# Kernel optimization log

Hardware: AMD Instinct MI355X
Metric: run time of the kernel (lower is better)

## Reference

```python
import jax, jax.numpy as jnp
import numpy as np

Z_SIZE, KEY_SIZE, HID = 128, 256, 512
NEG = -1e9


def setup_inputs() -> dict:
    key = jax.random.key(0)
    ks = jax.random.split(key, 8)
    B, T, H, W, Y = 512, 32, 32, 32, 4
    D = H * W
    g = lambda k, shape, s: jax.random.normal(k, shape, jnp.float32) * s
    return {
        "x_seq": jax.random.normal(ks[0], (B, T, H, W), jnp.float32),
        # Encoder (conv encoder stand-in: flatten -> MLP -> z_size)
        "enc_w1": g(ks[1], (D, HID), 0.03),
        "enc_b1": jnp.zeros((HID,), jnp.float32),
        "enc_w2": g(ks[2], (HID, Z_SIZE), 0.05),
        "enc_b2": jnp.zeros((Z_SIZE,), jnp.float32),
        # LSTM input kernel (recurrent kernel unused: h_prev is always 0)
        "lstm_Wx": g(ks[3], (KEY_SIZE + 1, 4 * HID), 0.05),
        "lstm_b": jnp.zeros((4 * HID,), jnp.float32),
        "keyw_W": g(ks[4], (HID, KEY_SIZE), 0.05),
        "keyw_b": jnp.zeros((KEY_SIZE,), jnp.float32),
        "g_W": g(ks[5], (HID, 1), 0.05),
        "g_b": jnp.zeros((1,), jnp.float32),
        "y_W": g(ks[6], (HID, Y), 0.05),
        "y_b": jnp.zeros((Y,), jnp.float32),
        "conf_gain": jnp.float32(1.0),
        "conf_bias": jnp.float32(0.0),
    }


def reference(x_seq, enc_w1, enc_b1, enc_w2, enc_b2, lstm_Wx, lstm_b,
              keyw_W, keyw_b, g_W, g_b, y_W, y_b, conf_gain, conf_bias):
    B, T = x_seq.shape[0], x_seq.shape[1]
    Y = y_b.shape[0]
    dt = x_seq.dtype

    # Encode all frames at once: (B, T, Z)
    x_flat = x_seq.reshape(B, T, -1)
    z_seq = jax.nn.relu(x_flat @ enc_w1 + enc_b1) @ enc_w2 + enc_b2
    # Pad with the zero z_t used at the final step t == T  -> (B, T+1, Z)
    z_pad = jnp.concatenate([z_seq, jnp.zeros((B, 1, Z_SIZE), dt)], axis=1)

    def lstm_step(x):  # single keras LSTM step from zero state (h=c=0)
        gates = x @ lstm_Wx + lstm_b
        i, f, c, o = jnp.split(gates, 4, axis=-1)  # keras gate order i,f,c,o
        c_new = jax.nn.sigmoid(i) * jnp.tanh(c)     # f*c_prev = 0
        return jax.nn.sigmoid(o) * jnp.tanh(c_new)

    slot_idx = jnp.arange(T + 1)

    def step(carry, t):
        key_r, M_k, M_v, _ = carry
        z_t = z_pad[:, t]                       # (B, Z)
        h = lstm_step(key_r)                    # (B, HID)
        key_w = h @ keyw_W + keyw_b             # (B, KEY)
        gate = jax.nn.sigmoid(h @ g_W + g_b)    # (B, 1)
        y_lin = h @ y_W + y_b                   # (B, Y)

        # Content-based read over memory slots written so far (slots < t)
        scores = jnp.einsum('bz,btz->bt', z_t, M_v)          # (B, T+1)
        valid = (slot_idx < t)[None, :]
        w_k = jax.nn.softmax(jnp.where(valid, scores, NEG), axis=1)
        c_k = jax.nn.sigmoid(scores * conf_gain + conf_bias)  # (B, T+1)
        Mkc = jnp.concatenate([M_k, c_k[..., None]], axis=-1)  # (B, T+1, KEY+1)
        key_r_new = gate * jnp.einsum('bt,btk->bk', w_k, Mkc)
        key_r_new = jnp.where(t == 0, jnp.zeros_like(key_r_new), key_r_new)

        # Memory write (append == write into preallocated slot t)
        M_k = M_k.at[:, t].set(key_w)
        M_v = M_v.at[:, t].set(z_t)
        return (key_r_new, M_k, M_v, y_lin), None

    init = (jnp.zeros((B, KEY_SIZE + 1), dt),
            jnp.zeros((B, T + 1, KEY_SIZE), dt),
            jnp.zeros((B, T + 1, Z_SIZE), dt),
            jnp.zeros((B, Y), dt))
    (_, _, _, y_pred_linear), _ = jax.lax.scan(step, init, jnp.arange(T + 1))
    y_pred = jnp.argmax(y_pred_linear, axis=1)
    return y_pred_linear, y_pred
```

## Files before the change

### kernel.cpp

```cpp
#include <hip/hip_runtime.h>
#include <math.h>

__device__ __forceinline__ float sigf(float x) { return 1.0f / (1.0f + expf(-x)); }
__device__ __forceinline__ float4 f4fma(float s, float4 b, float4 a) {
  return make_float4(fmaf(s, b.x, a.x), fmaf(s, b.y, a.y), fmaf(s, b.z, a.z), fmaf(s, b.w, a.w));
}
__device__ __forceinline__ void wave_red2(float4& v) {
  v.x += __shfl_xor(v.x, 16); v.y += __shfl_xor(v.y, 16);
  v.z += __shfl_xor(v.z, 16); v.w += __shfl_xor(v.w, 16);
  v.x += __shfl_xor(v.x, 32); v.y += __shfl_xor(v.y, 32);
  v.z += __shfl_xor(v.z, 32); v.w += __shfl_xor(v.w, 32);
}

__global__ __launch_bounds__(256) void k_gemm1(const float* __restrict__ X,
                                               const float* __restrict__ W,
                                               const float* __restrict__ Bv,
                                               float* __restrict__ C)
{
  const int K = 1024, N = 512;
  __shared__ float As[16][132];
  __shared__ float Bs[16][132];
  int tid = threadIdx.x;
  int bm = blockIdx.x >> 2;
  int bn = blockIdx.x & 3;
  int tx = tid & 15, ty = tid >> 4;
  int xr = tid & 127, xc8 = (tid >> 7) * 8;
  int wk = tid >> 4, wc = (tid & 15) * 8;
  const float* Xb = X + (size_t)(bm * 128 + xr) * K;
  const float* Wb = W + bn * 128 + wc;
  float acc[8][8];
#pragma unroll
  for (int i = 0; i < 8; i++)
#pragma unroll
    for (int j = 0; j < 8; j++) acc[i][j] = 0.f;

  for (int k0 = 0; k0 < K; k0 += 16) {
    float4 a0 = *(const float4*)(Xb + k0 + xc8);
    float4 a1 = *(const float4*)(Xb + k0 + xc8 + 4);
    float4 b0 = *(const float4*)(W + (size_t)(k0 + wk) * N + bn * 128 + wc);
    float4 b1 = *(const float4*)(W + (size_t)(k0 + wk) * N + bn * 128 + wc + 4);
    As[xc8 + 0][xr] = a0.x; As[xc8 + 1][xr] = a0.y;
    As[xc8 + 2][xr] = a0.z; As[xc8 + 3][xr] = a0.w;
    As[xc8 + 4][xr] = a1.x; As[xc8 + 5][xr] = a1.y;
    As[xc8 + 6][xr] = a1.z; As[xc8 + 7][xr] = a1.w;
    *(float4*)(&Bs[wk][wc]) = b0;
    *(float4*)(&Bs[wk][wc + 4]) = b1;
    __syncthreads();
#pragma unroll
    for (int kk = 0; kk < 16; kk++) {
      float a[8], b[8];
      *(float4*)(a)     = *(const float4*)(&As[kk][ty * 8]);
      *(float4*)(a + 4) = *(const float4*)(&As[kk][ty * 8 + 4]);
      *(float4*)(b)     = *(const float4*)(&Bs[kk][tx * 4]);
      *(float4*)(b + 4) = *(const float4*)(&Bs[kk][64 + tx * 4]);
#pragma unroll
      for (int i = 0; i < 8; i++)
#pragma unroll
        for (int j = 0; j < 8; j++) acc[i][j] = fmaf(a[i], b[j], acc[i][j]);
    }
    __syncthreads();
  }
  int crow0 = bm * 128 + ty * 8;
  int ccolA = bn * 128 + tx * 4;
  int ccolB = bn * 128 + 64 + tx * 4;
  float4 bvA = *(const float4*)(Bv + ccolA);
  float4 bvB = *(const float4*)(Bv + ccolB);
#pragma unroll
  for (int i = 0; i < 8; i++) {
    float4 vA = make_float4(acc[i][0] + bvA.x, acc[i][1] + bvA.y,
                            acc[i][2] + bvA.z, acc[i][3] + bvA.w);
    float4 vB = make_float4(acc[i][4] + bvB.x, acc[i][5] + bvB.y,
                            acc[i][6] + bvB.z, acc[i][7] + bvB.w);
    vA.x = vA.x > 0.f ? vA.x : 0.f; vA.y = vA.y > 0.f ? vA.y : 0.f;
    vA.z = vA.z > 0.f ? vA.z : 0.f; vA.w = vA.w > 0.f ? vA.w : 0.f;
    vB.x = vB.x > 0.f ? vB.x : 0.f; vB.y = vB.y > 0.f ? vB.y : 0.f;
    vB.z = vB.z > 0.f ? vB.z : 0.f; vB.w = vB.w > 0.f ? vB.w : 0.f;
    *(float4*)(&C[(size_t)(crow0 + i) * N + ccolA]) = vA;
    *(float4*)(&C[(size_t)(crow0 + i) * N + ccolB]) = vB;
  }
}

__global__ __launch_bounds__(256) void k_gemm2(const float* __restrict__ A,
                                               const float* __restrict__ W,
                                               const float* __restrict__ Bv,
                                               float* __restrict__ zp)
{
  const int K = 512, N = 128;
  __shared__ float As[8][132];
  __shared__ float Bs[8][132];
  int tid = threadIdx.x;
  int bm = blockIdx.x;
  int tx = tid & 15, ty = tid >> 4;
  int arow = tid >> 1, acol4 = (tid & 1) * 4;
  int bkk = tid >> 5, bn4 = (tid & 31) * 4;
  const float* Ab = A + (size_t)(bm * 128) * K;
  float acc[8][8];
#pragma unroll
  for (int i = 0; i < 8; i++)
#pragma unroll
    for (int j2 = 0; j2 < 8; j2++) acc[i][j2] = 0.f;
  for (int k0 = 0; k0 < K; k0 += 8) {
    float4 av = *(const float4*)(Ab + (size_t)arow * K + k0 + acol4);
    float4 bv = *(const float4*)(W + (size_t)(k0 + bkk) * N + bn4);
    As[acol4 + 0][arow] = av.x;
    As[acol4 + 1][arow] = av.y;
    As[acol4 + 2][arow] = av.z;
    As[acol4 + 3][arow] = av.w;
    *(float4*)(&Bs[bkk][bn4]) = bv;
    __syncthreads();
#pragma unroll
    for (int kk = 0; kk < 8; kk++) {
      float a[8], b[8];
      *(float4*)(a)     = *(const float4*)(&As[kk][ty * 8]);
      *(float4*)(a + 4) = *(const float4*)(&As[kk][ty * 8 + 4]);
      *(float4*)(b)     = *(const float4*)(&Bs[kk][tx * 8]);
      *(float4*)(b + 4) = *(const float4*)(&Bs[kk][tx * 8 + 4]);
#pragma unroll
      for (int i = 0; i < 8; i++)
#pragma unroll
        for (int j2 = 0; j2 < 8; j2++) acc[i][j2] = fmaf(a[i], b[j2], acc[i][j2]);
    }
    __syncthreads();
  }
  int ccol0 = tx * 8;
#pragma unroll
  for (int i = 0; i < 8; i++) {
    int r = bm * 128 + ty * 8 + i;
    int b = r >> 5, tt = r & 31;
#pragma unroll
    for (int j2 = 0; j2 < 8; j2++) {
      zp[(size_t)b * (33 * 128) + tt * 128 + ccol0 + j2] = acc[i][j2] + Bv[ccol0 + j2];
    }
  }
}

__global__ __launch_bounds__(256) void k_gram(const float* __restrict__ zp,
                                              float* __restrict__ warr,
                                              float* __restrict__ wc,
                                              const float* __restrict__ cgp,
                                              const float* __restrict__ cbp)
{
  __shared__ float zl[32][128];
  __shared__ float sg[32][32];
  int b = blockIdx.x, tid = threadIdx.x;
  const float* zb = zp + (size_t)b * (33 * 128);
  for (int i = tid; i < 32 * 128; i += 256) (&zl[0][0])[i] = zb[i];
  __syncthreads();
  for (int p = tid; p < 496; p += 256) {
    int t = 1;
    while (p >= t * (t + 1) / 2) t++;
    int tp = p - t * (t - 1) / 2;
    const float* za = &zl[t][0];
    const float* zc = &zl[tp][0];
    float s = 0.f;
#pragma unroll 4
    for (int c = 0; c < 128; c += 4) {
      s += za[c] * zc[c] + za[c + 1] * zc[c + 1] + za[c + 2] * zc[c + 2] + za[c + 3] * zc[c + 3];
    }
    sg[t][tp] = s;
  }
  __syncthreads();
  if (tid >= 1 && tid < 32) {
    int t = tid;
    float cg = cgp[0], cb = cbp[0];
    float m = -3.0e38f;
    for (int tp = 0; tp < t; tp++) m = fmaxf(m, sg[t][tp]);
    float se = 0.f;
    for (int tp = 0; tp < t; tp++) se += expf(sg[t][tp] - m);
    float inv = 1.0f / se;
    float wcs = 0.f;
    for (int tp = 0; tp < t; tp++) {
      float s = sg[t][tp];
      float w = expf(s - m) * inv;
      warr[(size_t)b * 1024 + t * 32 + tp] = w;
      wcs = fmaf(w, sigf(fmaf(s, cg, cb)), wcs);
    }
    wc[b * 32 + t] = wcs;
  }
}

__global__ __launch_bounds__(256) void k_gates(const float* __restrict__ Wx,
                                               const float* __restrict__ lb,
                                               const float* __restrict__ keyrT,
                                               float* __restrict__ h, int t)
{
  __shared__ float smem[6656];
  float* As = smem;
  float* Bs = smem + 640;
  float* Rb = smem;
  const int tid = threadIdx.x;
  const int rt = blockIdx.x >> 4;
  const int ct = blockIdx.x & 15;
  const int row0 = rt * 16;
  const int hc0 = ct * 32;

  if (t > 0) {
    const int ksub = tid >> 4;
    const int pos = tid & 15;
    const int rg = pos >> 3;
    const int cg = pos & 7;
    float4 aI[8], aC[8], aO[8];
#pragma unroll
    for (int r = 0; r < 8; r++) {
      aI[r] = make_float4(0.f, 0.f, 0.f, 0.f);
      aC[r] = make_float4(0.f, 0.f, 0.f, 0.f);
      aO[r] = make_float4(0.f, 0.f, 0.f, 0.f);
    }
    for (int c = 0; c < 8; ++c) {
      const int k0 = c * 32;
      if (c) __syncthreads();
      if (tid < 128) {
        const int kkA = tid >> 2, lA = (tid & 3) * 4;
        *(float4*)&As[kkA * 20 + lA] =
            *(const float4*)&keyrT[(size_t)(k0 + kkA) * 512 + row0 + lA];
      }
      {
        const int kkB = tid >> 3, lB = (tid & 7) * 4;
        const float* wrow = Wx + (size_t)(k0 + kkB) * 2048;
        *(float4*)&Bs[kkB * 100 + lB]      = *(const float4*)(wrow + hc0 + lB);
        *(float4*)&Bs[kkB * 100 + 32 + lB] = *(const float4*)(wrow + 1024 + hc0 + lB);
        *(float4*)&Bs[kkB * 100 + 64 + lB] = *(const float4*)(wrow + 1536 + hc0 + lB);
      }
      __syncthreads();
#pragma unroll
      for (int i = 0; i < 2; ++i) {
        const int kk = ksub * 2 + i;
        float a8[8];
        *(float4*)&a8[0] = *(const float4*)&As[kk * 20 + rg * 8];
        *(float4*)&a8[4] = *(const float4*)&As[kk * 20 + rg * 8 + 4];
        float4 bI = *(const float4*)&Bs[kk * 100 + cg * 4];
        float4 bC = *(const float4*)&Bs[kk * 100 + 32 + cg * 4];
        float4 bO = *(const float4*)&Bs[kk * 100 + 64 + cg * 4];
#pragma unroll
        for (int r = 0; r < 8; r++) {
          float a = a8[r];
          aI[r] = f4fma(a, bI, aI[r]);
          aC[r] = f4fma(a, bC, aC[r]);
          aO[r] = f4fma(a, bO, aO[r]);
        }
      }
    }
    if (ksub == 0) {
      float a8[8];
      *(float4*)&a8[0] = *(const float4*)&keyrT[(size_t)256 * 512 + row0 + rg * 8];
      *(float4*)&a8[4] = *(const float4*)&keyrT[(size_t)256 * 512 + row0 + rg * 8 + 4];
      const float* wrow = Wx + (size_t)256 * 2048;
      float4 bI = *(const float4*)(wrow + hc0 + cg * 4);
      float4 bC = *(const float4*)(wrow + 1024 + hc0 + cg * 4);
      float4 bO = *(const float4*)(wrow + 1536 + hc0 + cg * 4);
#pragma unroll
      for (int r = 0; r < 8; r++) {
        float a = a8[r];
        aI[r] = f4fma(a, bI, aI[r]);
        aC[r] = f4fma(a, bC, aC[r]);
        aO[r] = f4fma(a, bO, aO[r]);
      }
    }
#pragma unroll
    for (int r = 0; r < 8; r++) { wave_red2(aI[r]); wave_red2(aC[r]); wave_red2(aO[r]); }
    __syncthreads();
    {
      const int wave = tid >> 6, lane = tid & 63;
      if (lane < 16) {
        float* w = &Rb[wave * 1600 + lane * 100];
#pragma unroll
        for (int r = 0; r < 8; r++) {
          *(float4*)&w[r * 12 + 0] = aI[r];
          *(float4*)&w[r * 12 + 4] = aC[r];
          *(float4*)&w[r * 12 + 8] = aO[r];
        }
      }
    }
    __syncthreads();
    {
      const int r = tid >> 4;
      const int hc2 = (tid & 15) * 2;
      const int p = (r >> 3) * 8 + (hc2 >> 2);
      const int base = p * 100 + (r & 7) * 12;
      const int off = hc2 & 3;
      float sI0 = Rb[base + off]     + Rb[1600 + base + off]     + Rb[3200 + base + off]     + Rb[4800 + base + off];
      float sI1 = Rb[base + off + 1] + Rb[1600 + base + off + 1] + Rb[3200 + base + off + 1] + Rb[4800 + base + off + 1];
      float sC0 = Rb[base + 4 + off]     + Rb[1600 + base + 4 + off]     + Rb[3200 + base + 4 + off]     + Rb[4800 + base + 4 + off];
      float sC1 = Rb[base + 4 + off + 1] + Rb[1600 + base + 4 + off + 1] + Rb[3200 + base + 4 + off + 1] + Rb[4800 + base + 4 + off + 1];
      float sO0 = Rb[base + 8 + off]     + Rb[1600 + base + 8 + off]     + Rb[3200 + base + 8 + off]     + Rb[4800 + base + 8 + off];
      float sO1 = Rb[base + 8 + off + 1] + Rb[1600 + base + 8 + off + 1] + Rb[3200 + base + 8 + off + 1] + Rb[4800 + base + 8 + off + 1];
      float iv0 = sI0 + lb[hc0 + hc2],        iv1 = sI1 + lb[hc0 + hc2 + 1];
      float cv0 = sC0 + lb[1024 + hc0 + hc2], cv1 = sC1 + lb[1024 + hc0 + hc2 + 1];
      float ov0 = sO0 + lb[1536 + hc0 + hc2], ov1 = sO1 + lb[1536 + hc0 + hc2 + 1];
      float h0 = sigf(ov0) * tanhf(sigf(iv0) * tanhf(cv0));
      float h1 = sigf(ov1) * tanhf(sigf(iv1) * tanhf(cv1));
      *(float2*)&h[(size_t)(row0 + r) * 512 + hc0 + hc2] = make_float2(h0, h1);
    }
  } else {
    const int r = tid >> 4;
    const int hc2 = (tid & 15) * 2;
    float iv0 = lb[hc0 + hc2],        iv1 = lb[hc0 + hc2 + 1];
    float cv0 = lb[1024 + hc0 + hc2], cv1 = lb[1024 + hc0 + hc2 + 1];
    float ov0 = lb[1536 + hc0 + hc2], ov1 = lb[1536 + hc0 + hc2 + 1];
    float h0 = sigf(ov0) * tanhf(sigf(iv0) * tanhf(cv0));
    float h1 = sigf(ov1) * tanhf(sigf(iv1) * tanhf(cv1));
    *(float2*)&h[(size_t)(row0 + r) * 512 + hc0 + hc2] = make_float2(h0, h1);
  }
}

__global__ __launch_bounds__(256) void k_update(const float* __restrict__ h,
                                                const float* __restrict__ kW,
                                                const float* __restrict__ kb,
                                                const float* __restrict__ gW,
                                                const float* __restrict__ gb,
                                                const float* __restrict__ warr,
                                                const float* __restrict__ wc,
                                                float* __restrict__ Mk,
                                                float* __restrict__ keyrT, int t)
{
  __shared__ float smem[10640];
  float* hs  = smem;
  float* gWs = smem + 8256;
  float* wws = smem + 8768;
  float* gsh = smem + 9344;
  float* kWs = smem + 9360;
  float* Rb  = smem + 9360;
  const int tid = threadIdx.x;
  const int rt = blockIdx.x >> 4;
  const int ct = blockIdx.x & 15;
  const int row0 = rt * 16;
  const int c0 = ct * 16;

  {
    const int r = tid >> 4, seg = tid & 15;
    const float* hrow = h + (size_t)(row0 + r) * 512 + seg * 32;
    float* hd = hs + r * 516 + seg * 32;
#pragma unroll
    for (int q = 0; q < 8; ++q) {
      const int qp = ((q + seg) & 7) * 4;
      *(float4*)&hd[qp] = *(const float4*)&hrow[qp];
    }
    if (tid < 128) *(float4*)&gWs[tid * 4] = *(const float4*)&gW[tid * 4];
    wws[r * 36 + seg]      = (seg < t)      ? warr[(size_t)(row0 + r) * 1024 + t * 32 + seg] : 0.f;
    wws[r * 36 + 16 + seg] = (16 + seg < t) ? warr[(size_t)(row0 + r) * 1024 + t * 32 + 16 + seg] : 0.f;
  }
  __syncthreads();

  const int ksub = tid >> 4, pu = tid & 15, rgu = pu >> 2, cgu = pu & 3;
  float4 au[4];
#pragma unroll
  for (int r = 0; r < 4; r++) au[r] = make_float4(0.f, 0.f, 0.f, 0.f);
  for (int c = 0; c < 16; ++c) {
    if (c) __syncthreads();
    if (tid < 128) {
      const int kkW = tid >> 2, lW = (tid & 3) * 4;
      *(float4*)&kWs[kkW * 20 + lW] =
          *(const float4*)&kW[(size_t)(c * 32 + kkW) * 256 + c0 + lW];
    }
    __syncthreads();
#pragma unroll
    for (int i = 0; i < 2; ++i) {
      const int kk = ksub * 2 + i;
      float4 b4 = *(const float4*)&kWs[kk * 20 + cgu * 4];
      const int kidx = c * 32 + kk;
#pragma unroll
      for (int jj = 0; jj < 4; ++jj) {
        float a = hs[(rgu * 4 + jj) * 516 + kidx];
        au[jj] = f4fma(a, b4, au[jj]);
      }
    }
  }
#pragma unroll
  for (int r = 0; r < 4; r++) wave_red2(au[r]);
  __syncthreads();
  {
    const int wave = tid >> 6, lane = tid & 63;
    if (lane < 16) {
      float* w = &Rb[wave * 320 + lane * 20];
#pragma unroll
      for (int r = 0; r < 4; r++) *(float4*)&w[r * 4] = au[r];
    }
  }
  __syncthreads();
  {
    const int r = tid >> 4, cc = tid & 15;
    const int p = (r >> 2) * 4 + (cc >> 2);
    const int e = p * 20 + (r & 3) * 4 + (cc & 3);
    float v = Rb[e] + Rb[320 + e] + Rb[640 + e] + Rb[960 + e];
    Mk[(size_t)(row0 + r) * 8192 + t * 256 + c0 + cc] = v + kb[c0 + cc];
  }
  {
    const int r = tid >> 4, seg = tid & 15;
    const float* hp = &hs[r * 516 + seg * 32];
    const float* gp = &gWs[seg * 32];
    float s = 0.f;
#pragma unroll 8
    for (int j = 0; j < 32; ++j) s = fmaf(hp[j], gp[j], s);
    s += __shfl_xor(s, 1); s += __shfl_xor(s, 2);
    s += __shfl_xor(s, 4); s += __shfl_xor(s, 8);
    if (seg == 0) gsh[r] = sigf(s + gb[0]);
  }
  __syncthreads();
  {
    const int r = tid >> 4, cc = tid & 15;
    const int row = row0 + r;
    if (t == 0) {
      keyrT[(size_t)(c0 + cc) * 512 + row] = 0.f;
      if (ct == 0 && cc == 0) keyrT[(size_t)256 * 512 + row] = 0.f;
    } else {
      float a = 0.f;
      const float* mkb = Mk + (size_t)row * 8192 + c0 + cc;
      const float* wp = &wws[r * 36];
      for (int tp = 0; tp < t; ++tp) a = fmaf(wp[tp], mkb[tp * 256], a);
      float g = gsh[r];
      keyrT[(size_t)(c0 + cc) * 512 + row] = g * a;
      if (ct == 0 && cc == 0)
        keyrT[(size_t)256 * 512 + row] = g * wc[row * 32 + t];
    }
  }
}

__global__ __launch_bounds__(256) void k_y(const float* __restrict__ h,
                                           const float* __restrict__ yW,
                                           const float* __restrict__ yb,
                                           float* __restrict__ out)
{
  int tid = threadIdx.x;
  int wave = tid >> 6, lane = tid & 63;
  int row = blockIdx.x * 4 + wave;
  float a0 = 0.f, a1 = 0.f, a2 = 0.f, a3 = 0.f;
  for (int k = lane; k < 512; k += 64) {
    float hv = h[(size_t)row * 512 + k];
    float4 w4 = *(const float4*)(yW + k * 4);
    a0 = fmaf(hv, w4.x, a0);
    a1 = fmaf(hv, w4.y, a1);
    a2 = fmaf(hv, w4.z, a2);
    a3 = fmaf(hv, w4.w, a3);
  }
#pragma unroll
  for (int off = 32; off > 0; off >>= 1) {
    a0 += __shfl_xor(a0, off);
    a1 += __shfl_xor(a1, off);
    a2 += __shfl_xor(a2, off);
    a3 += __shfl_xor(a3, off);
  }
  if (lane == 0) {
    a0 += yb[0]; a1 += yb[1]; a2 += yb[2]; a3 += yb[3];
    out[row * 4 + 0] = a0;
    out[row * 4 + 1] = a1;
    out[row * 4 + 2] = a2;
    out[row * 4 + 3] = a3;
    int bi = 0; float bv = a0;
    if (a1 > bv) { bv = a1; bi = 1; }
    if (a2 > bv) { bv = a2; bi = 2; }
    if (a3 > bv) { bv = a3; bi = 3; }
    out[2048 + row] = (float)bi;
  }
}

extern "C" void kernel_launch(void* const* d_in, const int* in_sizes, int n_in,
                              void* d_out, int out_size, void* d_ws, size_t ws_size,
                              hipStream_t stream)
{
  const float* x  = (const float*)d_in[0];
  const float* w1 = (const float*)d_in[1];
  const float* b1 = (const float*)d_in[2];
  const float* w2 = (const float*)d_in[3];
  const float* b2 = (const float*)d_in[4];
  const float* Wx = (const float*)d_in[5];
  const float* lb = (const float*)d_in[6];
  const float* kW = (const float*)d_in[7];
  const float* kb = (const float*)d_in[8];
  const float* gW = (const float*)d_in[9];
  const float* gb = (const float*)d_in[10];
  const float* yW = (const float*)d_in[11];
  const float* yb = (const float*)d_in[12];
  const float* cg = (const float*)d_in[13];
  const float* cb = (const float*)d_in[14];
  float* out = (float*)d_out;
  char* ws = (char*)d_ws;
  float* C1    = (float*)(ws);
  float* Mk    = (float*)(ws);
  float* warr  = (float*)(ws + 16777216);
  float* wcb   = (float*)(ws + 18874368);
  float* keyrT = (float*)(ws + 18939904);
  float* h     = (float*)(ws + 19466240);
  float* zp    = (float*)(ws + 33554432);

  hipLaunchKernelGGL(k_gemm1, dim3(512), dim3(256), 0, stream, x, w1, b1, C1);
  hipLaunchKernelGGL(k_gemm2, dim3(128), dim3(256), 0, stream, C1, w2, b2, zp);
  hipLaunchKernelGGL(k_gram, dim3(512), dim3(256), 0, stream, zp, warr, wcb, cg, cb);
  for (int t = 0; t <= 32; t++) {
    hipLaunchKernelGGL(k_gates, dim3(512), dim3(256), 0, stream, Wx, lb, keyrT, h, t);
    if (t < 32) {
      hipLaunchKernelGGL(k_update, dim3(512), dim3(256), 0, stream,
                         h, kW, kb, gW, gb, warr, wcb, Mk, keyrT, t);
    }
  }
  hipLaunchKernelGGL(k_y, dim3(128), dim3(256), 0, stream, h, yW, yb, out);
}
```

Baseline: 1.320 ms.

## Retile GEMMs and gate kernels with smaller tiles, more blocks, register prefetch

The encoder GEMMs use smaller output tiles (64x128 and 32x128), which gives more blocks for the 256 CUs, and gemm1 now prefetches the next K-slice into registers while computing. The LSTM gates kernel moves to 16-column tiles across 1024 blocks with a 64-wide K chunk and register prefetch, adding one more shuffle stage to the reduction. The key-update kernel doubles its K chunk and prefetches weights. The aim is better occupancy and overlap of global loads with math in both the per-step recurrent kernels and the one-time GEMMs. In exchange, each tile does less arithmetic per load and more blocks re-read the same weights.

After: 1.431 ms. 8.4% more time.

```diff
diff --git a/kernel.cpp b/kernel.cpp
--- a/kernel.cpp
+++ b/kernel.cpp
@@ -5,12 +5,17 @@
 __device__ __forceinline__ float4 f4fma(float s, float4 b, float4 a) {
   return make_float4(fmaf(s, b.x, a.x), fmaf(s, b.y, a.y), fmaf(s, b.z, a.z), fmaf(s, b.w, a.w));
 }
-__device__ __forceinline__ void wave_red2(float4& v) {
+__device__ __forceinline__ void wave_red16_32(float4& v) {
   v.x += __shfl_xor(v.x, 16); v.y += __shfl_xor(v.y, 16);
   v.z += __shfl_xor(v.z, 16); v.w += __shfl_xor(v.w, 16);
   v.x += __shfl_xor(v.x, 32); v.y += __shfl_xor(v.y, 32);
   v.z += __shfl_xor(v.z, 32); v.w += __shfl_xor(v.w, 32);
 }
+__device__ __forceinline__ void wave_red8_16_32(float4& v) {
+  v.x += __shfl_xor(v.x, 8);  v.y += __shfl_xor(v.y, 8);
+  v.z += __shfl_xor(v.z, 8);  v.w += __shfl_xor(v.w, 8);
+  wave_red16_32(v);
+}
 
 __global__ __launch_bounds__(256) void k_gemm1(const float* __restrict__ X,
                                                const float* __restrict__ W,
@@ -18,63 +23,87 @@
                                                float* __restrict__ C)
 {
   const int K = 1024, N = 512;
-  __shared__ float As[16][132];
-  __shared__ float Bs[16][132];
-  int tid = threadIdx.x;
-  int bm = blockIdx.x >> 2;
-  int bn = blockIdx.x & 3;
-  int tx = tid & 15, ty = tid >> 4;
-  int xr = tid & 127, xc8 = (tid >> 7) * 8;
-  int wk = tid >> 4, wc = (tid & 15) * 8;
-  const float* Xb = X + (size_t)(bm * 128 + xr) * K;
+  __shared__ float As[32][68];
+  __shared__ float Bs[32][132];
+  const int tid = threadIdx.x;
+  const int bm = blockIdx.x >> 2;
+  const int bn = blockIdx.x & 3;
+  const int ty = tid >> 4, tx = tid & 15;
+  const int ar = tid & 63, ac4 = (tid >> 6) * 4;
+  const int wk = tid >> 3, wc = (tid & 7) * 16;
+  const float* Xb = X + (size_t)(bm * 64 + ar) * K;
   const float* Wb = W + bn * 128 + wc;
-  float acc[8][8];
-#pragma unroll
-  for (int i = 0; i < 8; i++)
+  float acc[4][8];
+#pragma unroll
+  for (int i = 0; i < 4; i++)
 #pragma unroll
     for (int j = 0; j < 8; j++) acc[i][j] = 0.f;
 
-  for (int k0 = 0; k0 < K; k0 += 16) {
-    float4 a0 = *(const float4*)(Xb + k0 + xc8);
-    float4 a1 = *(const float4*)(Xb + k0 + xc8 + 4);
-    float4 b0 = *(const float4*)(W + (size_t)(k0 + wk) * N + bn * 128 + wc);
-    float4 b1 = *(const float4*)(W + (size_t)(k0 + wk) * N + bn * 128 + wc + 4);
-    As[xc8 + 0][xr] = a0.x; As[xc8 + 1][xr] = a0.y;
-    As[xc8 + 2][xr] = a0.z; As[xc8 + 3][xr] = a0.w;
-    As[xc8 + 4][xr] = a1.x; As[xc8 + 5][xr] = a1.y;
-    As[xc8 + 6][xr] = a1.z; As[xc8 + 7][xr] = a1.w;
-    *(float4*)(&Bs[wk][wc]) = b0;
-    *(float4*)(&Bs[wk][wc + 4]) = b1;
+  float4 pa0, pa1, pw0, pw1, pw2, pw3;
+  {
+    pa0 = *(const float4*)(Xb + ac4);
+    pa1 = *(const float4*)(Xb + ac4 + 16);
+    const float* wr = Wb + (size_t)wk * N;
+    pw0 = *(const float4*)(wr);
+    pw1 = *(const float4*)(wr + 4);
+    pw2 = *(const float4*)(wr + 8);
+    pw3 = *(const float4*)(wr + 12);
+  }
+  for (int k0 = 0; k0 < K; k0 += 32) {
+    if (k0) __syncthreads();
+    As[ac4 + 0][ar] = pa0.x; As[ac4 + 1][ar] = pa0.y;
+    As[ac4 + 2][ar] = pa0.z; As[ac4 + 3][ar] = pa0.w;
+    As[ac4 + 16][ar] = pa1.x; As[ac4 + 17][ar] = pa1.y;
+    As[ac4 + 18][ar] = pa1.z; As[ac4 + 19][ar] = pa1.w;
+    *(float4*)(&Bs[wk][wc])      = pw0;
+    *(float4*)(&Bs[wk][wc + 4])  = pw1;
+    *(float4*)(&Bs[wk][wc + 8])  = pw2;
+    *(float4*)(&Bs[wk][wc + 12]) = pw3;
     __syncthreads();
-#pragma unroll
-    for (int kk = 0; kk < 16; kk++) {
-      float a[8], b[8];
-      *(float4*)(a)     = *(const float4*)(&As[kk][ty * 8]);
-      *(float4*)(a + 4) = *(const float4*)(&As[kk][ty * 8 + 4]);
-      *(float4*)(b)     = *(const float4*)(&Bs[kk][tx * 4]);
-      *(float4*)(b + 4) = *(const float4*)(&Bs[kk][64 + tx * 4]);
-#pragma unroll
-      for (int i = 0; i < 8; i++)
-#pragma unroll
-        for (int j = 0; j < 8; j++) acc[i][j] = fmaf(a[i], b[j], acc[i][j]);
-    }
-    __syncthreads();
-  }
-  int crow0 = bm * 128 + ty * 8;
-  int ccolA = bn * 128 + tx * 4;
-  int ccolB = bn * 128 + 64 + tx * 4;
+    if (k0 < K - 32) {
+      const int kn = k0 + 32;
+      pa0 = *(const float4*)(Xb + kn + ac4);
+      pa1 = *(const float4*)(Xb + kn + ac4 + 16);
+      const float* wr = Wb + (size_t)(kn + wk) * N;
+      pw0 = *(const float4*)(wr);
+      pw1 = *(const float4*)(wr + 4);
+      pw2 = *(const float4*)(wr + 8);
+      pw3 = *(const float4*)(wr + 12);
+    }
+#pragma unroll
+    for (int kk = 0; kk < 32; kk++) {
+      float4 a = *(const float4*)(&As[kk][ty * 4]);
+      float4 bA = *(const float4*)(&Bs[kk][tx * 4]);
+      float4 bB = *(const float4*)(&Bs[kk][64 + tx * 4]);
+      float ar4[4] = {a.x, a.y, a.z, a.w};
+#pragma unroll
+      for (int i = 0; i < 4; i++) {
+        acc[i][0] = fmaf(ar4[i], bA.x, acc[i][0]);
+        acc[i][1] = fmaf(ar4[i], bA.y, acc[i][1]);
+        acc[i][2] = fmaf(ar4[i], bA.z, acc[i][2]);
+        acc[i][3] = fmaf(ar4[i], bA.w, acc[i][3]);
+        acc[i][4] = fmaf(ar4[i], bB.x, acc[i][4]);
+        acc[i][5] = fmaf(ar4[i], bB.y, acc[i][5]);
+        acc[i][6] = fmaf(ar4[i], bB.z, acc[i][6]);
+        acc[i][7] = fmaf(ar4[i], bB.w, acc[i][7]);
+      }
+    }
+  }
+  const int crow0 = bm * 64 + ty * 4;
+  const int ccolA = bn * 128 + tx * 4;
+  const int ccolB = ccolA + 64;
   float4 bvA = *(const float4*)(Bv + ccolA);
   float4 bvB = *(const float4*)(Bv + ccolB);
 #pragma unroll
-  for (int i = 0; i < 8; i++) {
+  for (int i = 0; i < 4; i++) {
     float4 vA = make_float4(acc[i][0] + bvA.x, acc[i][1] + bvA.y,
                             acc[i][2] + bvA.z, acc[i][3] + bvA.w);
     float4 vB = make_float4(acc[i][4] + bvB.x, acc[i][5] + bvB.y,
                             acc[i][6] + bvB.z, acc[i][7] + bvB.w);
-    vA.x = vA.x > 0.f ? vA.x : 0.f; vA.y = vA.y > 0.f ? vA.y : 0.f;
-    vA.z = vA.z > 0.f ? vA.z : 0.f; vA.w = vA.w > 0.f ? vA.w : 0.f;
-    vB.x = vB.x > 0.f ? vB.x : 0.f; vB.y = vB.y > 0.f ? vB.y : 0.f;
-    vB.z = vB.z > 0.f ? vB.z : 0.f; vB.w = vB.w > 0.f ? vB.w : 0.f;
+    vA.x = fmaxf(vA.x, 0.f); vA.y = fmaxf(vA.y, 0.f);
+    vA.z = fmaxf(vA.z, 0.f); vA.w = fmaxf(vA.w, 0.f);
+    vB.x = fmaxf(vB.x, 0.f); vB.y = fmaxf(vB.y, 0.f);
+    vB.z = fmaxf(vB.z, 0.f); vB.w = fmaxf(vB.w, 0.f);
     *(float4*)(&C[(size_t)(crow0 + i) * N + ccolA]) = vA;
     *(float4*)(&C[(size_t)(crow0 + i) * N + ccolB]) = vB;
   }
@@ -86,51 +115,57 @@
                                                float* __restrict__ zp)
 {
   const int K = 512, N = 128;
-  __shared__ float As[8][132];
-  __shared__ float Bs[8][132];
-  int tid = threadIdx.x;
-  int bm = blockIdx.x;
-  int tx = tid & 15, ty = tid >> 4;
-  int arow = tid >> 1, acol4 = (tid & 1) * 4;
-  int bkk = tid >> 5, bn4 = (tid & 31) * 4;
-  const float* Ab = A + (size_t)(bm * 128) * K;
-  float acc[8][8];
-#pragma unroll
-  for (int i = 0; i < 8; i++)
-#pragma unroll
-    for (int j2 = 0; j2 < 8; j2++) acc[i][j2] = 0.f;
-  for (int k0 = 0; k0 < K; k0 += 8) {
-    float4 av = *(const float4*)(Ab + (size_t)arow * K + k0 + acol4);
-    float4 bv = *(const float4*)(W + (size_t)(k0 + bkk) * N + bn4);
-    As[acol4 + 0][arow] = av.x;
-    As[acol4 + 1][arow] = av.y;
-    As[acol4 + 2][arow] = av.z;
-    As[acol4 + 3][arow] = av.w;
-    *(float4*)(&Bs[bkk][bn4]) = bv;
+  __shared__ float As[16][36];
+  __shared__ float Bs[16][132];
+  const int tid = threadIdx.x;
+  const int bm = blockIdx.x;
+  const int ty = tid >> 4, tx = tid & 15;
+  const int ar = tid & 31, ac4 = ((tid >> 5) & 3) * 4;
+  const int bk = tid >> 4, bc8 = (tid & 15) * 8;
+  float acc[2][8];
+#pragma unroll
+  for (int i = 0; i < 2; i++)
+#pragma unroll
+    for (int j = 0; j < 8; j++) acc[i][j] = 0.f;
+
+  for (int k0 = 0; k0 < K; k0 += 16) {
+    if (tid < 128) {
+      float4 av = *(const float4*)(A + (size_t)(bm * 32 + ar) * K + k0 + ac4);
+      As[ac4 + 0][ar] = av.x; As[ac4 + 1][ar] = av.y;
+      As[ac4 + 2][ar] = av.z; As[ac4 + 3][ar] = av.w;
+    }
+    *(float4*)(&Bs[bk][bc8]) = *(const float4*)(W + (size_t)(k0 + bk) * N + bc8);
+    *(float4*)(&Bs[bk][bc8 + 4]) = *(const float4*)(W + (size_t)(k0 + bk) * N + bc8 + 4);
     __syncthreads();
 #pragma unroll
-    for (int kk = 0; kk < 8; kk++) {
-      float a[8], b[8];
-      *(float4*)(a)     = *(const float4*)(&As[kk][ty * 8]);
-      *(float4*)(a + 4) = *(const float4*)(&As[kk][ty * 8 + 4]);
-      *(float4*)(b)     = *(const float4*)(&Bs[kk][tx * 8]);
-      *(float4*)(b + 4) = *(const float4*)(&Bs[kk][tx * 8 + 4]);
-#pragma unroll
-      for (int i = 0; i < 8; i++)
-#pragma unroll
-        for (int j2 = 0; j2 < 8; j2++) acc[i][j2] = fmaf(a[i], b[j2], acc[i][j2]);
+    for (int kk = 0; kk < 16; kk++) {
+      float a0 = As[kk][ty * 2], a1 = As[kk][ty * 2 + 1];
+      float4 bA = *(const float4*)(&Bs[kk][tx * 4]);
+      float4 bB = *(const float4*)(&Bs[kk][64 + tx * 4]);
+      acc[0][0] = fmaf(a0, bA.x, acc[0][0]); acc[0][1] = fmaf(a0, bA.y, acc[0][1]);
+      acc[0][2] = fmaf(a0, bA.z, acc[0][2]); acc[0][3] = fmaf(a0, bA.w, acc[0][3]);
+      acc[0][4] = fmaf(a0, bB.x, acc[0][4]); acc[0][5] = fmaf(a0, bB.y, acc[0][5]);
+      acc[0][6] = fmaf(a0, bB.z, acc[0][6]); acc[0][7] = fmaf(a0, bB.w, acc[0][7]);
+      acc[1][0] = fmaf(a1, bA.x, acc[1][0]); acc[1][1] = fmaf(a1, bA.y, acc[1][1]);
+      acc[1][2] = fmaf(a1, bA.z, acc[1][2]); acc[1][3] = fmaf(a1, bA.w, acc[1][3]);
+      acc[1][4] = fmaf(a1, bB.x, acc[1][4]); acc[1][5] = fmaf(a1, bB.y, acc[1][5]);
+      acc[1][6] = fmaf(a1, bB.z, acc[1][6]); acc[1][7] = fmaf(a1, bB.w, acc[1][7]);
     }
     __syncthreads();
   }
-  int ccol0 = tx * 8;
-#pragma unroll
-  for (int i = 0; i < 8; i++) {
-    int r = bm * 128 + ty * 8 + i;
+  const int ccolA = tx * 4, ccolB = ccolA + 64;
+  float4 bvA = *(const float4*)(Bv + ccolA);
+  float4 bvB = *(const float4*)(Bv + ccolB);
+#pragma unroll
+  for (int i = 0; i < 2; i++) {
+    int r = bm * 32 + ty * 2 + i;
     int b = r >> 5, tt = r & 31;
-#pragma unroll
-    for (int j2 = 0; j2 < 8; j2++) {
-      zp[(size_t)b * (33 * 128) + tt * 128 + ccol0 + j2] = acc[i][j2] + Bv[ccol0 + j2];
-    }
+    float4 vA = make_float4(acc[i][0] + bvA.x, acc[i][1] + bvA.y,
+                            acc[i][2] + bvA.z, acc[i][3] + bvA.w);
+    float4 vB = make_float4(acc[i][4] + bvB.x, acc[i][5] + bvB.y,
+                            acc[i][6] + bvB.z, acc[i][7] + bvB.w);
+    *(float4*)(&zp[(size_t)b * 4096 + tt * 128 + ccolA]) = vA;
+    *(float4*)(&zp[(size_t)b * 4096 + tt * 128 + ccolB]) = vB;
   }
 }
 
@@ -143,7 +178,7 @@
   __shared__ float zl[32][128];
   __shared__ float sg[32][32];
   int b = blockIdx.x, tid = threadIdx.x;
-  const float* zb = zp + (size_t)b * (33 * 128);
+  const float* zb = zp + (size_t)b * 4096;
   for (int i = tid; i < 32 * 128; i += 256) (&zl[0][0])[i] = zb[i];
   __syncthreads();
   for (int p = tid; p < 496; p += 256) {
@@ -184,21 +219,23 @@
                                                const float* __restrict__ keyrT,
                                                float* __restrict__ h, int t)
 {
-  __shared__ float smem[6656];
+  __shared__ float smem[4608];
   float* As = smem;
-  float* Bs = smem + 640;
+  float* Bs = smem + 1280;
   float* Rb = smem;
   const int tid = threadIdx.x;
-  const int rt = blockIdx.x >> 4;
-  const int ct = blockIdx.x & 15;
+  const int rt = blockIdx.x >> 5;
+  const int ct = blockIdx.x & 31;
   const int row0 = rt * 16;
-  const int hc0 = ct * 32;
+  const int hc0 = ct * 16;
 
   if (t > 0) {
-    const int ksub = tid >> 4;
-    const int pos = tid & 15;
-    const int rg = pos >> 3;
-    const int cg = pos & 7;
+    const int ksub = tid >> 3;
+    const int pos = tid & 7;
+    const int rg = pos >> 2;
+    const int cg = pos & 3;
+    const int kkS = tid >> 2;
+    const int lS = (tid & 3) * 4;
     float4 aI[8], aC[8], aO[8];
 #pragma unroll
     for (int r = 0; r < 8; r++) {
@@ -206,31 +243,38 @@
       aC[r] = make_float4(0.f, 0.f, 0.f, 0.f);
       aO[r] = make_float4(0.f, 0.f, 0.f, 0.f);
     }
-    for (int c = 0; c < 8; ++c) {
-      const int k0 = c * 32;
+    float4 pA, pB0, pB1, pB2;
+    {
+      pA = *(const float4*)&keyrT[(size_t)kkS * 512 + row0 + lS];
+      const float* wrow = Wx + (size_t)kkS * 2048 + hc0 + lS;
+      pB0 = *(const float4*)(wrow);
+      pB1 = *(const float4*)(wrow + 1024);
+      pB2 = *(const float4*)(wrow + 1536);
+    }
+    for (int c = 0; c < 4; ++c) {
       if (c) __syncthreads();
-      if (tid < 128) {
-        const int kkA = tid >> 2, lA = (tid & 3) * 4;
-        *(float4*)&As[kkA * 20 + lA] =
-            *(const float4*)&keyrT[(size_t)(k0 + kkA) * 512 + row0 + lA];
+      *(float4*)&As[kkS * 20 + lS] = pA;
+      *(float4*)&Bs[kkS * 52 + lS] = pB0;
+      *(float4*)&Bs[kkS * 52 + 16 + lS] = pB1;
+      *(float4*)&Bs[kkS * 52 + 32 + lS] = pB2;
+      __syncthreads();
+      if (c < 3) {
+        const int kn = (c + 1) * 64 + kkS;
+        pA = *(const float4*)&keyrT[(size_t)kn * 512 + row0 + lS];
+        const float* wrow = Wx + (size_t)kn * 2048 + hc0 + lS;
+        pB0 = *(const float4*)(wrow);
+        pB1 = *(const float4*)(wrow + 1024);
+        pB2 = *(const float4*)(wrow + 1536);
       }
-      {
-        const int kkB = tid >> 3, lB = (tid & 7) * 4;
-        const float* wrow = Wx + (size_t)(k0 + kkB) * 2048;
-        *(float4*)&Bs[kkB * 100 + lB]      = *(const float4*)(wrow + hc0 + lB);
-        *(float4*)&Bs[kkB * 100 + 32 + lB] = *(const float4*)(wrow + 1024 + hc0 + lB);
-        *(float4*)&Bs[kkB * 100 + 64 + lB] = *(const float4*)(wrow + 1536 + hc0 + lB);
-      }
-      __syncthreads();
 #pragma unroll
       for (int i = 0; i < 2; ++i) {
         const int kk = ksub * 2 + i;
         float a8[8];
         *(float4*)&a8[0] = *(const float4*)&As[kk * 20 + rg * 8];
         *(float4*)&a8[4] = *(const float4*)&As[kk * 20 + rg * 8 + 4];
-        float4 bI = *(const float4*)&Bs[kk * 100 + cg * 4];
-        float4 bC = *(const float4*)&Bs[kk * 100 + 32 + cg * 4];
-        float4 bO = *(const float4*)&Bs[kk * 100 + 64 + cg * 4];
+        float4 bI = *(const float4*)&Bs[kk * 52 + cg * 4];
+        float4 bC = *(const float4*)&Bs[kk * 52 + 16 + cg * 4];
+        float4 bO = *(const float4*)&Bs[kk * 52 + 32 + cg * 4];
 #pragma unroll
         for (int r = 0; r < 8; r++) {
           float a = a8[r];
@@ -240,14 +284,14 @@
         }
       }
     }
-    if (ksub == 0) {
+    if (tid < 8) {
       float a8[8];
       *(float4*)&a8[0] = *(const float4*)&keyrT[(size_t)256 * 512 + row0 + rg * 8];
       *(float4*)&a8[4] = *(const float4*)&keyrT[(size_t)256 * 512 + row0 + rg * 8 + 4];
-      const float* wrow = Wx + (size_t)256 * 2048;
-      float4 bI = *(const float4*)(wrow + hc0 + cg * 4);
-      float4 bC = *(const float4*)(wrow + 1024 + hc0 + cg * 4);
-      float4 bO = *(const float4*)(wrow + 1536 + hc0 + cg * 4);
+      const float* wrow = Wx + (size_t)256 * 2048 + hc0 + cg * 4;
+      float4 bI = *(const float4*)(wrow);
+      float4 bC = *(const float4*)(wrow + 1024);
+      float4 bO = *(const float4*)(wrow + 1536);
 #pragma unroll
       for (int r = 0; r < 8; r++) {
         float a = a8[r];
@@ -257,12 +301,12 @@
       }
     }
 #pragma unroll
-    for (int r = 0; r < 8; r++) { wave_red2(aI[r]); wave_red2(aC[r]); wave_red2(aO[r]); }
+    for (int r = 0; r < 8; r++) { wave_red8_16_32(aI[r]); wave_red8_16_32(aC[r]); wave_red8_16_32(aO[r]); }
     __syncthreads();
     {
       const int wave = tid >> 6, lane = tid & 63;
-      if (lane < 16) {
-        float* w = &Rb[wave * 1600 + lane * 100];
+      if (lane < 8) {
+        float* w = &Rb[wave * 800 + lane * 100];
 #pragma unroll
         for (int r = 0; r < 8; r++) {
           *(float4*)&w[r * 12 + 0] = aI[r];
@@ -274,32 +318,22 @@
     __syncthreads();
     {
       const int r = tid >> 4;
-      const int hc2 = (tid & 15) * 2;
-      const int p = (r >> 3) * 8 + (hc2 >> 2);
-      const int base = p * 100 + (r & 7) * 12;
-      const int off = hc2 & 3;
-      float sI0 = Rb[base + off]     + Rb[1600 + base + off]     + Rb[3200 + base + off]     + Rb[4800 + base + off];
-      float sI1 = Rb[base + off + 1] + Rb[1600 + base + off + 1] + Rb[3200 + base + off + 1] + Rb[4800 + base + off + 1];
-      float sC0 = Rb[base + 4 + off]     + Rb[1600 + base + 4 + off]     + Rb[3200 + base + 4 + off]     + Rb[4800 + base + 4 + off];
-      float sC1 = Rb[base + 4 + off + 1] + Rb[1600 + base + 4 + off + 1] + Rb[3200 + base + 4 + off + 1] + Rb[4800 + base + 4 + off + 1];
-      float sO0 = Rb[base + 8 + off]     + Rb[1600 + base + 8 + off]     + Rb[3200 + base + 8 + off]     + Rb[4800 + base + 8 + off];
-      float sO1 = Rb[base + 8 + off + 1] + Rb[1600 + base + 8 + off + 1] + Rb[3200 + base + 8 + off + 1] + Rb[4800 + base + 8 + off + 1];
-      float iv0 = sI0 + lb[hc0 + hc2],        iv1 = sI1 + lb[hc0 + hc2 + 1];
-      float cv0 = sC0 + lb[1024 + hc0 + hc2], cv1 = sC1 + lb[1024 + hc0 + hc2 + 1];
-      float ov0 = sO0 + lb[1536 + hc0 + hc2], ov1 = sO1 + lb[1536 + hc0 + hc2 + 1];
-      float h0 = sigf(ov0) * tanhf(sigf(iv0) * tanhf(cv0));
-      float h1 = sigf(ov1) * tanhf(sigf(iv1) * tanhf(cv1));
-      *(float2*)&h[(size_t)(row0 + r) * 512 + hc0 + hc2] = make_float2(h0, h1);
+      const int hc = tid & 15;
+      const int p = (r >> 3) * 4 + (hc >> 2);
+      const int base = p * 100 + (r & 7) * 12 + (hc & 3);
+      float sI = Rb[base]     + Rb[800 + base]     + Rb[1600 + base]     + Rb[2400 + base];
+      float sC = Rb[base + 4] + Rb[800 + base + 4] + Rb[1600 + base + 4] + Rb[2400 + base + 4];
+      float sO = Rb[base + 8] + Rb[800 + base + 8] + Rb[1600 + base + 8] + Rb[2400 + base + 8];
+      float iv = sI + lb[hc0 + hc];
+      float cv = sC + lb[1024 + hc0 + hc];
+      float ov = sO + lb[1536 + hc0 + hc];
+      h[(size_t)(row0 + r) * 512 + hc0 + hc] = sigf(ov) * tanhf(sigf(iv) * tanhf(cv));
     }
   } else {
     const int r = tid >> 4;
-    const int hc2 = (tid & 15) * 2;
-    float iv0 = lb[hc0 + hc2],        iv1 = lb[hc0 + hc2 + 1];
-    float cv0 = lb[1024 + hc0 + hc2], cv1 = lb[1024 + hc0 + hc2 + 1];
-    float ov0 = lb[1536 + hc0 + hc2], ov1 = lb[1536 + hc0 + hc2 + 1];
-    float h0 = sigf(ov0) * tanhf(sigf(iv0) * tanhf(cv0));
-    float h1 = sigf(ov1) * tanhf(sigf(iv1) * tanhf(cv1));
-    *(float2*)&h[(size_t)(row0 + r) * 512 + hc0 + hc2] = make_float2(h0, h1);
+    const int hc = tid & 15;
+    float hv = sigf(lb[1536 + hc0 + hc]) * tanhf(sigf(lb[hc0 + hc]) * tanhf(lb[1024 + hc0 + hc]));
+    h[(size_t)(row0 + r) * 512 + hc0 + hc] = hv;
   }
 }
 
@@ -339,25 +373,24 @@
     wws[r * 36 + seg]      = (seg < t)      ? warr[(size_t)(row0 + r) * 1024 + t * 32 + seg] : 0.f;
     wws[r * 36 + 16 + seg] = (16 + seg < t) ? warr[(size_t)(row0 + r) * 1024 + t * 32 + 16 + seg] : 0.f;
   }
+  const int kkW = tid >> 2, lW = (tid & 3) * 4;
+  float4 pW = *(const float4*)&kW[(size_t)kkW * 256 + c0 + lW];
   __syncthreads();
 
   const int ksub = tid >> 4, pu = tid & 15, rgu = pu >> 2, cgu = pu & 3;
   float4 au[4];
 #pragma unroll
   for (int r = 0; r < 4; r++) au[r] = make_float4(0.f, 0.f, 0.f, 0.f);
-  for (int c = 0; c < 16; ++c) {
+  for (int c = 0; c < 8; ++c) {
     if (c) __syncthreads();
-    if (tid < 128) {
-      const int kkW = tid >> 2, lW = (tid & 3) * 4;
-      *(float4*)&kWs[kkW * 20 + lW] =
-          *(const float4*)&kW[(size_t)(c * 32 + kkW) * 256 + c0 + lW];
-    }
+    *(float4*)&kWs[kkW * 20 + lW] = pW;
     __syncthreads();
-#pragma unroll
-    for (int i = 0; i < 2; ++i) {
-      const int kk = ksub * 2 + i;
+    if (c < 7) pW = *(const float4*)&kW[(size_t)((c + 1) * 64 + kkW) * 256 + c0 + lW];
+#pragma unroll
+    for (int i = 0; i < 4; ++i) {
+      const int kk = ksub * 4 + i;
       float4 b4 = *(const float4*)&kWs[kk * 20 + cgu * 4];
-      const int kidx = c * 32 + kk;
+      const int kidx = c * 64 + kk;
 #pragma unroll
       for (int jj = 0; jj < 4; ++jj) {
         float a = hs[(rgu * 4 + jj) * 516 + kidx];
@@ -366,7 +399,7 @@
     }
   }
 #pragma unroll
-  for (int r = 0; r < 4; r++) wave_red2(au[r]);
+  for (int r = 0; r < 4; r++) wave_red16_32(au[r]);
   __syncthreads();
   {
     const int wave = tid >> 6, lane = tid & 63;
@@ -482,11 +515,11 @@
   float* h     = (float*)(ws + 19466240);
   float* zp    = (float*)(ws + 33554432);
 
-  hipLaunchKernelGGL(k_gemm1, dim3(512), dim3(256), 0, stream, x, w1, b1, C1);
-  hipLaunchKernelGGL(k_gemm2, dim3(128), dim3(256), 0, stream, C1, w2, b2, zp);
+  hipLaunchKernelGGL(k_gemm1, dim3(1024), dim3(256), 0, stream, x, w1, b1, C1);
+  hipLaunchKernelGGL(k_gemm2, dim3(512), dim3(256), 0, stream, C1, w2, b2, zp);
   hipLaunchKernelGGL(k_gram, dim3(512), dim3(256), 0, stream, zp, warr, wcb, cg, cb);
   for (int t = 0; t <= 32; t++) {
-    hipLaunchKernelGGL(k_gates, dim3(512), dim3(256), 0, stream, Wx, lb, keyrT, h, t);
+    hipLaunchKernelGGL(k_gates, dim3(1024), dim3(256), 0, stream, Wx, lb, keyrT, h, t);
     if (t < 32) {
       hipLaunchKernelGGL(k_update, dim3(512), dim3(256), 0, stream,
                          h, kW, kb, gW, gb, warr, wcb, Mk, keyrT, t);
```
